# Kernel optimization log

Hardware: AMD Instinct MI355X
Metric: run time of the kernel (lower is better)

## Reference

```python
import jax, jax.numpy as jnp
import numpy as np

N_NODES = 2048
N_EDGES = 32768
N_IN = 256
MSG_HID = 512
MSG_OUT = 256
N_HID = 512


def _linear_params(key, fan_in, fan_out):
    kw, kb = jax.random.split(key)
    bound = 1.0 / np.sqrt(fan_in)
    W = jax.random.uniform(kw, (fan_out, fan_in), jnp.float32, -bound, bound)
    b = jax.random.uniform(kb, (fan_out,), jnp.float32, -bound, bound)
    return W, b


def setup_inputs() -> dict:
    key = jax.random.key(0)
    ks = jax.random.split(key, 8)
    inputs = jax.random.normal(ks[0], (N_NODES, N_IN), jnp.float32)
    # one-hot incidence matrices built from random receiver/sender node indices
    recv_idx = jax.random.randint(ks[1], (N_EDGES,), 0, N_NODES)
    send_idx = jax.random.randint(ks[2], (N_EDGES,), 0, N_NODES)
    rel_rec = jax.nn.one_hot(recv_idx, N_NODES, dtype=jnp.float32)   # [E, N]
    rel_send = jax.nn.one_hot(send_idx, N_NODES, dtype=jnp.float32)  # [E, N]
    msg_W1, msg_b1 = _linear_params(ks[3], 2 * N_IN, MSG_HID)
    msg_W2, msg_b2 = _linear_params(ks[4], MSG_HID, MSG_OUT)
    out_W1, out_b1 = _linear_params(ks[5], N_IN + MSG_OUT, N_HID)
    out_W2, out_b2 = _linear_params(ks[6], N_HID, N_HID)
    out_W3, out_b3 = _linear_params(ks[7], N_HID, N_IN)
    return {
        'inputs': inputs, 'rel_rec': rel_rec, 'rel_send': rel_send,
        'msg_W1': msg_W1, 'msg_b1': msg_b1, 'msg_W2': msg_W2, 'msg_b2': msg_b2,
        'out_W1': out_W1, 'out_b1': out_b1, 'out_W2': out_W2, 'out_b2': out_b2,
        'out_W3': out_W3, 'out_b3': out_b3,
    }


def reference(inputs, rel_rec, rel_send, msg_W1, msg_b1, msg_W2, msg_b2,
              out_W1, out_b1, out_W2, out_b2, out_W3, out_b3):
    # gather node features to edges via dense one-hot matmuls (as in original)
    receivers = rel_rec @ inputs    # [E, n_in]
    senders = rel_send @ inputs     # [E, n_in]
    pre_msg = jnp.concatenate([senders, receivers], axis=1)  # [E, 2*n_in]
    # edge-message MLP (dropout p=0 -> identity)
    msg = jax.nn.relu(pre_msg @ msg_W1.T + msg_b1)
    msg = jax.nn.relu(msg @ msg_W2.T + msg_b2)               # [E, msg_out]
    # scatter-add messages to receiving nodes: (msg^T @ rel_rec)^T == rel_rec^T @ msg
    agg_msgs = rel_rec.T @ msg                               # [N, msg_out]
    aug_inputs = jnp.concatenate([inputs, agg_msgs], axis=-1)
    # node-update MLP
    pred = jax.nn.relu(aug_inputs @ out_W1.T + out_b1)
    pred = jax.nn.relu(pred @ out_W2.T + out_b2)
    pred = pred @ out_W3.T + out_b3
    return inputs + pred
```

## Files before the change

### kernel.cpp

```cpp
#include <hip/hip_runtime.h>
#include <hip/hip_bf16.h>
#include <stdint.h>

using bf16 = __hip_bfloat16;
typedef short bf16x8 __attribute__((ext_vector_type(8)));
typedef float floatx4 __attribute__((ext_vector_type(4)));

static constexpr int NODES = 2048;
static constexpr int EDGES = 32768;

__device__ inline uint4 cvt8(const float* __restrict__ p) {
    const float4* f = (const float4*)p;
    float4 a = f[0], b = f[1];
    union { uint4 u; bf16 h[8]; } pk;
    pk.h[0] = __float2bfloat16(a.x); pk.h[1] = __float2bfloat16(a.y);
    pk.h[2] = __float2bfloat16(a.z); pk.h[3] = __float2bfloat16(a.w);
    pk.h[4] = __float2bfloat16(b.x); pk.h[5] = __float2bfloat16(b.y);
    pk.h[6] = __float2bfloat16(b.z); pk.h[7] = __float2bfloat16(b.w);
    return pk.u;
}

__global__ __launch_bounds__(256) void zero_agg(float4* __restrict__ p) {
    p[(size_t)blockIdx.x * 256 + threadIdx.x] = float4{0.f, 0.f, 0.f, 0.f};
}

__global__ __launch_bounds__(256) void extract_idx(
    const float* __restrict__ rel_rec, const float* __restrict__ rel_send,
    int* __restrict__ recv_idx, int* __restrict__ send_idx)
{
    const int b = blockIdx.x;
    const int half = b >> 13;
    const int rb = b & 8191;
    const float* mat = half ? rel_send : rel_rec;
    int* out = half ? send_idx : recv_idx;
    const int w = threadIdx.x >> 6;
    const int lane = threadIdx.x & 63;
    const int row = rb * 4 + w;
    if (lane == 0) out[row] = 0;
    const uint4* base = (const uint4*)(mat + (size_t)row * NODES);
    for (int p = 0; p < 8; ++p) {
        uint4 v = base[p * 64 + lane];
        const bool hit = (v.x | v.y | v.z | v.w) != 0u;
        if (hit) {
            int e = v.x ? 0 : (v.y ? 1 : (v.z ? 2 : 3));
            out[row] = p * 256 + lane * 4 + e;
        }
        if (__any(hit)) break;
    }
}

template<int AMODE, int EPI>
__global__ __launch_bounds__(256, 2) void gemm128(
    const bf16* __restrict__ A, const float* __restrict__ Bt,
    const float* __restrict__ bias, bf16* __restrict__ Cout,
    float* __restrict__ OutF, const float* __restrict__ inputsF,
    const int* __restrict__ sidx, const int* __restrict__ ridx,
    const float* __restrict__ aggin, float* __restrict__ aggout,
    int M, int N, int K)
{
    constexpr int BM = 128, BN = 128, BK = 32;
    __shared__ bf16 As[BM * BK];
    __shared__ bf16 Bs[BN * BK];
    __shared__ int sIdx[BM];
    __shared__ int rIdx[BM];

    const int t = threadIdx.x;
    const int m0 = blockIdx.y * BM;
    const int n0 = blockIdx.x * BN;

    if constexpr (AMODE == 1) {
        if (t < BM) {
            sIdx[t] = sidx[m0 + t] & (NODES - 1);
            rIdx[t] = ridx[m0 + t] & (NODES - 1);
        }
        __syncthreads();
    }

    const int sr = t >> 2;
    const int sc = t & 3;

    uint4 ra[2], rb[2];

    auto loadTiles = [&](int kt) {
        const int kk = kt * BK + sc * 8;
#pragma unroll
        for (int p = 0; p < 2; ++p) {
            const int row = p * 64 + sr;
            if constexpr (AMODE == 0) {
                ra[p] = *(const uint4*)(A + (size_t)(m0 + row) * K + kk);
            } else if constexpr (AMODE == 1) {
                const int node = (kk < 256) ? sIdx[row] : rIdx[row];
                ra[p] = cvt8(inputsF + (size_t)node * 256 + (kk & 255));
            } else {
                const float* src = (kk < 256)
                    ? (inputsF + (size_t)(m0 + row) * 256 + kk)
                    : (aggin + (size_t)(m0 + row) * 256 + (kk - 256));
                ra[p] = cvt8(src);
            }
            rb[p] = cvt8(Bt + (size_t)(n0 + row) * K + kk);
        }
    };

    const int wv = t >> 6;
    const int lane = t & 63;
    const int wm = wv >> 1, wn = wv & 1;
    const int r16 = lane & 15, q = lane >> 4;

    floatx4 acc[4][4] = {};

    loadTiles(0);
    const int KT = K / BK;
    for (int kt = 0; kt < KT; ++kt) {
        __syncthreads();
#pragma unroll
        for (int p = 0; p < 2; ++p) {
            *(uint4*)(&As[(p * 64 + sr) * BK + sc * 8]) = ra[p];
            *(uint4*)(&Bs[(p * 64 + sr) * BK + sc * 8]) = rb[p];
        }
        __syncthreads();
        if (kt + 1 < KT) loadTiles(kt + 1);

        bf16x8 af[4], bf[4];
#pragma unroll
        for (int i = 0; i < 4; ++i)
            af[i] = *(const bf16x8*)(&As[(wm * 64 + i * 16 + r16) * BK + q * 8]);
#pragma unroll
        for (int j = 0; j < 4; ++j)
            bf[j] = *(const bf16x8*)(&Bs[(wn * 64 + j * 16 + r16) * BK + q * 8]);
#pragma unroll
        for (int i = 0; i < 4; ++i)
#pragma unroll
            for (int j = 0; j < 4; ++j)
                acc[i][j] = __builtin_amdgcn_mfma_f32_16x16x32_bf16(af[i], bf[j], acc[i][j], 0, 0, 0);
    }

    float bv[4];
#pragma unroll
    for (int j = 0; j < 4; ++j)
        bv[j] = bias[n0 + wn * 64 + j * 16 + r16];

#pragma unroll
    for (int i = 0; i < 4; ++i) {
        const int rbase = m0 + wm * 64 + i * 16 + q * 4;
#pragma unroll
        for (int j = 0; j < 4; ++j) {
            const int gc = n0 + wn * 64 + j * 16 + r16;
#pragma unroll
            for (int r = 0; r < 4; ++r) {
                float v = acc[i][j][r] + bv[j];
                const int gr = rbase + r;
                if constexpr (EPI == 0) {
                    v = fmaxf(v, 0.0f);
                    Cout[(size_t)gr * N + gc] = __float2bfloat16(v);
                } else if constexpr (EPI == 1) {
                    v = fmaxf(v, 0.0f);
                    atomicAdd(&aggout[(size_t)(ridx[gr] & (NODES - 1)) * 256 + gc], v);
                } else {
                    OutF[(size_t)gr * 256 + gc] = inputsF[(size_t)gr * 256 + gc] + v;
                }
            }
        }
    }
}

extern "C" void kernel_launch(void* const* d_in, const int* in_sizes, int n_in,
                              void* d_out, int out_size, void* d_ws, size_t ws_size,
                              hipStream_t stream) {
    const float* inputs   = (const float*)d_in[0];
    const float* rel_rec  = (const float*)d_in[1];
    const float* rel_send = (const float*)d_in[2];
    const float* msg_W1   = (const float*)d_in[3];
    const float* msg_b1   = (const float*)d_in[4];
    const float* msg_W2   = (const float*)d_in[5];
    const float* msg_b2   = (const float*)d_in[6];
    const float* out_W1   = (const float*)d_in[7];
    const float* out_b1   = (const float*)d_in[8];
    const float* out_W2   = (const float*)d_in[9];
    const float* out_b2   = (const float*)d_in[10];
    const float* out_W3   = (const float*)d_in[11];
    const float* out_b3   = (const float*)d_in[12];

    char* ws = (char*)d_ws;
    int*   recv_idx = (int*)(ws + 0);
    int*   send_idx = (int*)(ws + 131072);
    float* agg      = (float*)(ws + 262144);
    bf16*  g1       = (bf16*)(ws + 2359296);
    bf16*  g2       = (bf16*)(ws + 4456448);
    bf16*  h1       = (bf16*)(ws + 6553600);
    const size_t fixed = 6553600;

    int EC;
    if      (ws_size >= fixed + (size_t)32768 * 512 * 2) EC = 32768;
    else if (ws_size >= fixed + (size_t)8192  * 512 * 2) EC = 8192;
    else if (ws_size >= fixed + (size_t)2048  * 512 * 2) EC = 2048;
    else return;

    extract_idx<<<16384, 256, 0, stream>>>(rel_rec, rel_send, recv_idx, send_idx);

    zero_agg<<<512, 256, 0, stream>>>((float4*)agg);

    for (int e0 = 0; e0 < EDGES; e0 += EC) {
        gemm128<1, 0><<<dim3(512 / 128, EC / 128), 256, 0, stream>>>(
            nullptr, msg_W1, msg_b1, h1, nullptr, inputs,
            send_idx + e0, recv_idx + e0, nullptr, nullptr, EC, 512, 512);
        gemm128<0, 1><<<dim3(256 / 128, EC / 128), 256, 0, stream>>>(
            h1, msg_W2, msg_b2, nullptr, nullptr, nullptr,
            nullptr, recv_idx + e0, nullptr, agg, EC, 256, 512);
    }

    gemm128<2, 0><<<dim3(512 / 128, NODES / 128), 256, 0, stream>>>(
        nullptr, out_W1, out_b1, g1, nullptr, inputs,
        nullptr, nullptr, agg, nullptr, NODES, 512, 512);

    gemm128<0, 0><<<dim3(512 / 128, NODES / 128), 256, 0, stream>>>(
        g1, out_W2, out_b2, g2, nullptr, nullptr,
        nullptr, nullptr, nullptr, nullptr, NODES, 512, 512);

    gemm128<0, 2><<<dim3(256 / 128, NODES / 128), 256, 0, stream>>>(
        g2, out_W3, out_b3, nullptr, (float*)d_out, inputs,
        nullptr, nullptr, nullptr, nullptr, NODES, 256, 512);
}
```

Baseline: 645.4 us.

## Precompute per-node first-layer projections and fuse edge gather into second GEMM

```diff
diff --git a/kernel.cpp b/kernel.cpp
--- a/kernel.cpp
+++ b/kernel.cpp
@@ -49,14 +49,15 @@
     }
 }
 
-template<int AMODE, int EPI>
+template<int AMODE, int BMODE, int EPI>
 __global__ __launch_bounds__(256, 2) void gemm128(
-    const bf16* __restrict__ A, const float* __restrict__ Bt,
-    const float* __restrict__ bias, bf16* __restrict__ Cout,
-    float* __restrict__ OutF, const float* __restrict__ inputsF,
-    const int* __restrict__ sidx, const int* __restrict__ ridx,
-    const float* __restrict__ aggin, float* __restrict__ aggout,
-    int M, int N, int K)
+    const bf16* __restrict__ A, const float* __restrict__ Af,
+    const float* __restrict__ Bt, const float* __restrict__ bias,
+    bf16* __restrict__ Cout, float* __restrict__ OutF,
+    const float* __restrict__ inputsF, const float* __restrict__ UV,
+    const float* __restrict__ b1v, const int* __restrict__ sidx,
+    const int* __restrict__ ridx, const float* __restrict__ aggin,
+    float* __restrict__ aggout, int M, int N, int K)
 {
     constexpr int BM = 128, BN = 128, BK = 32;
     __shared__ bf16 As[BM * BK];
@@ -68,7 +69,7 @@
     const int m0 = blockIdx.y * BM;
     const int n0 = blockIdx.x * BN;
 
-    if constexpr (AMODE == 1) {
+    if constexpr (AMODE == 3) {
         if (t < BM) {
             sIdx[t] = sidx[m0 + t] & (NODES - 1);
             rIdx[t] = ridx[m0 + t] & (NODES - 1);
@@ -89,15 +90,34 @@
             if constexpr (AMODE == 0) {
                 ra[p] = *(const uint4*)(A + (size_t)(m0 + row) * K + kk);
             } else if constexpr (AMODE == 1) {
-                const int node = (kk < 256) ? sIdx[row] : rIdx[row];
-                ra[p] = cvt8(inputsF + (size_t)node * 256 + (kk & 255));
-            } else {
+                ra[p] = cvt8(Af + (size_t)(m0 + row) * K + kk);
+            } else if constexpr (AMODE == 2) {
                 const float* src = (kk < 256)
                     ? (inputsF + (size_t)(m0 + row) * 256 + kk)
                     : (aggin + (size_t)(m0 + row) * 256 + (kk - 256));
                 ra[p] = cvt8(src);
+            } else {
+                const float4* u = (const float4*)(UV + (size_t)sIdx[row] * 1024 + kk);
+                const float4* v = (const float4*)(UV + (size_t)rIdx[row] * 1024 + 512 + kk);
+                const float4* c = (const float4*)(b1v + kk);
+                float4 u0 = u[0], u1 = u[1], v0 = v[0], v1 = v[1], c0 = c[0], c1 = c[1];
+                union { uint4 q; bf16 h[8]; } pk;
+                pk.h[0] = __float2bfloat16(fmaxf(u0.x + v0.x + c0.x, 0.f));
+                pk.h[1] = __float2bfloat16(fmaxf(u0.y + v0.y + c0.y, 0.f));
+                pk.h[2] = __float2bfloat16(fmaxf(u0.z + v0.z + c0.z, 0.f));
+                pk.h[3] = __float2bfloat16(fmaxf(u0.w + v0.w + c0.w, 0.f));
+                pk.h[4] = __float2bfloat16(fmaxf(u1.x + v1.x + c1.x, 0.f));
+                pk.h[5] = __float2bfloat16(fmaxf(u1.y + v1.y + c1.y, 0.f));
+                pk.h[6] = __float2bfloat16(fmaxf(u1.z + v1.z + c1.z, 0.f));
+                pk.h[7] = __float2bfloat16(fmaxf(u1.w + v1.w + c1.w, 0.f));
+                ra[p] = pk.q;
             }
-            rb[p] = cvt8(Bt + (size_t)(n0 + row) * K + kk);
+            if constexpr (BMODE == 0) {
+                rb[p] = cvt8(Bt + (size_t)(n0 + row) * K + kk);
+            } else {
+                const int n = n0 + row;
+                rb[p] = cvt8(Bt + (size_t)(n & 511) * 512 + (n >> 9) * 256 + kk);
+            }
         }
     };
 
@@ -120,24 +140,24 @@
         __syncthreads();
         if (kt + 1 < KT) loadTiles(kt + 1);
 
-        bf16x8 af[4], bf[4];
+        bf16x8 af[4], bfr[4];
 #pragma unroll
         for (int i = 0; i < 4; ++i)
             af[i] = *(const bf16x8*)(&As[(wm * 64 + i * 16 + r16) * BK + q * 8]);
 #pragma unroll
         for (int j = 0; j < 4; ++j)
-            bf[j] = *(const bf16x8*)(&Bs[(wn * 64 + j * 16 + r16) * BK + q * 8]);
+            bfr[j] = *(const bf16x8*)(&Bs[(wn * 64 + j * 16 + r16) * BK + q * 8]);
 #pragma unroll
         for (int i = 0; i < 4; ++i)
 #pragma unroll
             for (int j = 0; j < 4; ++j)
-                acc[i][j] = __builtin_amdgcn_mfma_f32_16x16x32_bf16(af[i], bf[j], acc[i][j], 0, 0, 0);
+                acc[i][j] = __builtin_amdgcn_mfma_f32_16x16x32_bf16(af[i], bfr[j], acc[i][j], 0, 0, 0);
     }
 
     float bv[4];
 #pragma unroll
     for (int j = 0; j < 4; ++j)
-        bv[j] = bias[n0 + wn * 64 + j * 16 + r16];
+        bv[j] = (EPI == 3) ? 0.f : bias[n0 + wn * 64 + j * 16 + r16];
 
 #pragma unroll
     for (int i = 0; i < 4; ++i) {
@@ -154,9 +174,11 @@
                     Cout[(size_t)gr * N + gc] = __float2bfloat16(v);
                 } else if constexpr (EPI == 1) {
                     v = fmaxf(v, 0.0f);
-                    atomicAdd(&aggout[(size_t)(ridx[gr] & (NODES - 1)) * 256 + gc], v);
+                    atomicAdd(&aggout[(size_t)rIdx[gr - m0] * 256 + gc], v);
+                } else if constexpr (EPI == 2) {
+                    OutF[(size_t)gr * 256 + gc] = inputsF[(size_t)gr * 256 + gc] + v;
                 } else {
-                    OutF[(size_t)gr * 256 + gc] = inputsF[(size_t)gr * 256 + gc] + v;
+                    OutF[(size_t)gr * N + gc] = v;
                 }
             }
         }
@@ -184,39 +206,37 @@
     int*   recv_idx = (int*)(ws + 0);
     int*   send_idx = (int*)(ws + 131072);
     float* agg      = (float*)(ws + 262144);
-    bf16*  g1       = (bf16*)(ws + 2359296);
-    bf16*  g2       = (bf16*)(ws + 4456448);
-    bf16*  h1       = (bf16*)(ws + 6553600);
-    const size_t fixed = 6553600;
-
-    int EC;
-    if      (ws_size >= fixed + (size_t)32768 * 512 * 2) EC = 32768;
-    else if (ws_size >= fixed + (size_t)8192  * 512 * 2) EC = 8192;
-    else if (ws_size >= fixed + (size_t)2048  * 512 * 2) EC = 2048;
-    else return;
+    float* UV       = (float*)(ws + 2359296);
+    bf16*  g1       = (bf16*)(ws + 10747904);
+    bf16*  g2       = (bf16*)(ws + 12845056);
+    if (ws_size < (size_t)15 * 1024 * 1024) return;
 
     extract_idx<<<16384, 256, 0, stream>>>(rel_rec, rel_send, recv_idx, send_idx);
 
     zero_agg<<<512, 256, 0, stream>>>((float4*)agg);
 
-    for (int e0 = 0; e0 < EDGES; e0 += EC) {
-        gemm128<1, 0><<<dim3(512 / 128, EC / 128), 256, 0, stream>>>(
-            nullptr, msg_W1, msg_b1, h1, nullptr, inputs,
-            send_idx + e0, recv_idx + e0, nullptr, nullptr, EC, 512, 512);
-        gemm128<0, 1><<<dim3(256 / 128, EC / 128), 256, 0, stream>>>(
-            h1, msg_W2, msg_b2, nullptr, nullptr, nullptr,
-            nullptr, recv_idx + e0, nullptr, agg, EC, 256, 512);
-    }
-
-    gemm128<2, 0><<<dim3(512 / 128, NODES / 128), 256, 0, stream>>>(
-        nullptr, out_W1, out_b1, g1, nullptr, inputs,
-        nullptr, nullptr, agg, nullptr, NODES, 512, 512);
-
-    gemm128<0, 0><<<dim3(512 / 128, NODES / 128), 256, 0, stream>>>(
-        g1, out_W2, out_b2, g2, nullptr, nullptr,
-        nullptr, nullptr, nullptr, nullptr, NODES, 512, 512);
-
-    gemm128<0, 2><<<dim3(256 / 128, NODES / 128), 256, 0, stream>>>(
-        g2, out_W3, out_b3, nullptr, (float*)d_out, inputs,
-        nullptr, nullptr, nullptr, nullptr, NODES, 256, 512);
-}
+    gemm128<1, 1, 3><<<dim3(1024 / 128, NODES / 128), 256, 0, stream>>>(
+        nullptr, inputs, msg_W1, nullptr, nullptr, UV,
+        nullptr, nullptr, nullptr, nullptr, nullptr, nullptr, nullptr,
+        NODES, 1024, 256);
+
+    gemm128<3, 0, 1><<<dim3(256 / 128, EDGES / 128), 256, 0, stream>>>(
+        nullptr, nullptr, msg_W2, msg_b2, nullptr, nullptr,
+        nullptr, UV, msg_b1, send_idx, recv_idx, nullptr, agg,
+        EDGES, 256, 512);
+
+    gemm128<2, 0, 0><<<dim3(512 / 128, NODES / 128), 256, 0, stream>>>(
+        nullptr, nullptr, out_W1, out_b1, g1, nullptr,
+        inputs, nullptr, nullptr, nullptr, nullptr, agg, nullptr,
+        NODES, 512, 512);
+
+    gemm128<0, 0, 0><<<dim3(512 / 128, NODES / 128), 256, 0, stream>>>(
+        g1, nullptr, out_W2, out_b2, g2, nullptr,
+        nullptr, nullptr, nullptr, nullptr, nullptr, nullptr, nullptr,
+        NODES, 512, 512);
+
+    gemm128<0, 0, 2><<<dim3(256 / 128, NODES / 128), 256, 0, stream>>>(
+        g2, nullptr, out_W3, out_b3, nullptr, (float*)d_out,
+        inputs, nullptr, nullptr, nullptr, nullptr, nullptr, nullptr,
+        NODES, 256, 512);
+}
```

Result: faster. 628.9 us (-2.6%).
